# Performance work log

Hardware: AMD Instinct MI355X
Metric: run time of the kernel (lower is better)

The kernel has to match this reference:

```python
import jax, jax.numpy as jnp
import numpy as np

B, T, D, E = 4, 1024, 1024, 8
HD = 4 * D  # hdim = 4*dim


def setup_inputs() -> dict:
    key = jax.random.key(0)
    k1, k2, k3, k4 = jax.random.split(key, 4)
    std = 0.5 * D ** (-0.5)
    bound = (3.0 ** 0.5) * std
    x = jax.random.normal(k1, (B, T, D), dtype=jnp.float32)
    # router zero-init in source; use small random weights so routing is non-degenerate
    router_w = jax.random.normal(k2, (E, D), dtype=jnp.float32) * 0.02
    expert_fc = jax.random.uniform(k3, (E, D, HD), dtype=jnp.float32, minval=-bound, maxval=bound)
    # proj zero-init in source; use small random so output/backward are non-trivial
    expert_proj = jax.random.normal(k4, (E, D, HD), dtype=jnp.float32) * 0.02
    return {"x": x, "router_w": router_w, "expert_fc": expert_fc, "expert_proj": expert_proj}


def reference(x, router_w, expert_fc, expert_proj):
    # router: Linear(dim, E, bias=False) -> logits [B,T,E]
    logits = jnp.einsum('btd,ed->bte', x, router_w)
    probs = jax.nn.softmax(logits, axis=-1)
    expert_ids = jnp.argmax(probs, axis=-1)  # [B,T]; top-1 (max) routing
    # NOTE: source computes expert_weights (max prob) but does NOT use it in combine.
    mask = jax.nn.one_hot(expert_ids, E, dtype=x.dtype)  # [B,T,E]
    # Dense all-experts compute (faithful to source): h = x @ fc (F.linear with fc.T)
    h = jnp.einsum('btd,edh->ebth', x, expert_fc)
    h = jnp.square(jax.nn.relu(h))  # relu(h)**2
    # expert_output = h @ proj.T (F.linear with proj [dim, hdim])
    out_e = jnp.einsum('ebth,edh->ebtd', h, expert_proj)
    # masked combine: sum_e out_e * (ids == e)
    output = jnp.einsum('ebtd,bte->btd', out_e, mask)
    return output
```

## Files before the change

kernel.cpp:

```cpp
#include <hip/hip_runtime.h>
#include <hip/hip_bf16.h>
#include <stdint.h>

#define NE 8
#define DIM 1024
#define HDIM 4096
#define NTOK 4096
#define KSPLIT 4
#define MAXT 24
#define NT 16

typedef unsigned short ushort_t;
typedef __attribute__((ext_vector_type(4))) float f32x4;
typedef __attribute__((ext_vector_type(8))) short bf16x8;
typedef __attribute__((ext_vector_type(8))) ushort_t u16x8;

#define WAITV(n) asm volatile("s_waitcnt vmcnt(" #n ")" ::: "memory")
#define WAITL0() asm volatile("s_waitcnt lgkmcnt(0)" ::: "memory")
#define WAITL8() asm volatile("s_waitcnt lgkmcnt(8)" ::: "memory")
#define SCHEDB() __builtin_amdgcn_sched_barrier(0)
#define BARRIER() __builtin_amdgcn_s_barrier()

__device__ __forceinline__ ushort_t f2b(float f) {
  union { float f; unsigned u; } c; c.f = f;
  unsigned u = c.u;
  return (ushort_t)((u + 0x7fffu + ((u >> 16) & 1u)) >> 16);
}

__device__ __forceinline__ void gl2lds16(const void* g, void* l) {
  __builtin_amdgcn_global_load_lds(
      (__attribute__((address_space(1))) void*)g,
      (__attribute__((address_space(3))) void*)l, 16, 0, 0);
}

#define PH_MFMA(mh, nh)                                                     \
  { __builtin_amdgcn_s_setprio(1);                                          \
    _Pragma("unroll")                                                       \
    for (int i2 = 0; i2 < 4; ++i2) {                                        \
      _Pragma("unroll")                                                     \
      for (int j2 = 0; j2 < 2; ++j2) {                                      \
        _Pragma("unroll")                                                   \
        for (int kk = 0; kk < 2; ++kk)                                      \
          acc[(mh)*4 + i2][(nh)*2 + j2] =                                   \
            __builtin_amdgcn_mfma_f32_16x16x32_bf16(                        \
              af[i2][kk], bf[(nh)*2 + j2][kk],                              \
              acc[(mh)*4 + i2][(nh)*2 + j2], 0, 0, 0);                      \
      }                                                                     \
    }                                                                       \
    __builtin_amdgcn_s_setprio(0); }

#define LOAD_AF(mh)                                                         \
  { _Pragma("unroll")                                                       \
    for (int i2 = 0; i2 < 4; ++i2) {                                        \
      _Pragma("unroll")                                                     \
      for (int kk = 0; kk < 2; ++kk)                                        \
        af[i2][kk] = *(const bf16x8*)&pA[aBase + ((mh)*64 + i2*16)*64 + ck[kk]]; \
    } }
#define LOAD_BF(nh)                                                         \
  { _Pragma("unroll")                                                       \
    for (int j2 = 0; j2 < 2; ++j2) {                                        \
      _Pragma("unroll")                                                     \
      for (int kk = 0; kk < 2; ++kk)                                        \
        bf[(nh)*2 + j2][kk] = *(const bf16x8*)&pB[bBase + (((nh)*2 + j2)*16)*64 + ck[kk]]; \
    } }

__global__ __launch_bounds__(256) void router_kernel(
    const float* __restrict__ x, const float* __restrict__ rw,
    int* __restrict__ eid, int* __restrict__ rank, int* __restrict__ cnt) {
  __shared__ float w[NE * 1028];
  for (int i = threadIdx.x; i < NE * DIM; i += 256) {
    int e = i >> 10, d = i & 1023;
    w[e * 1028 + d] = rw[i];
  }
  __syncthreads();
  int grp = threadIdx.x >> 3;
  int e = threadIdx.x & 7;
  int t = blockIdx.x * 32 + grp;
  const float4* xr = (const float4*)(x + (size_t)t * DIM);
  const float4* wr = (const float4*)(w + e * 1028);
  float acc = 0.f;
#pragma unroll 4
  for (int i = 0; i < DIM / 4; ++i) {
    float4 xv = xr[i], wv = wr[i];
    acc += xv.x * wv.x + xv.y * wv.y + xv.z * wv.z + xv.w * wv.w;
  }
  float v = acc; int ie = e;
#pragma unroll
  for (int m = 4; m; m >>= 1) {
    float ov = __shfl_xor(v, m, 8);
    int oi = __shfl_xor(ie, m, 8);
    if (ov > v || (ov == v && oi < ie)) { v = ov; ie = oi; }
  }
  if (e == 0) {
    eid[t] = ie;
    rank[t] = atomicAdd(&cnt[ie], 1);
  }
}

__global__ void scan_kernel(const int* __restrict__ cnt, int* __restrict__ offs,
                            int* __restrict__ tile_e, int* __restrict__ tile_m,
                            int* __restrict__ ntiles) {
  if (threadIdx.x == 0) {
    int s = 0, nt = 0;
    for (int e = 0; e < NE; ++e) {
      offs[e] = s;
      int c = cnt[e];
      for (int m = 0; m < c; m += 256) { tile_e[nt] = e; tile_m[nt] = m; ++nt; }
      s += c;
    }
    offs[NE] = s;
    *ntiles = nt;
  }
}

__global__ __launch_bounds__(256) void gather_kernel(
    const float* __restrict__ x, const int* __restrict__ eid,
    const int* __restrict__ rank, const int* __restrict__ offs,
    int* __restrict__ sorted, ushort_t* __restrict__ Xg) {
  int t = blockIdx.x;
  int e = eid[t];
  int pos = offs[e] + rank[t];
  if (threadIdx.x == 0) sorted[pos] = t;
  int i = threadIdx.x;
  float4 v = ((const float4*)(x + (size_t)t * DIM))[i];
  ushort4 o = make_ushort4(f2b(v.x), f2b(v.y), f2b(v.z), f2b(v.w));
  *(ushort4*)(Xg + (size_t)pos * DIM + i * 4) = o;
}

__global__ __launch_bounds__(256) void transpose_fc_kernel(
    const float* __restrict__ fc, ushort_t* __restrict__ fct) {
  __shared__ float tile[64][68];
  int e = blockIdx.z;
  int h0 = blockIdx.x * 64, d0 = blockIdx.y * 64;
  int tid = threadIdx.x;
  int rr = tid >> 4;
  int cc = (tid & 15) * 4;
  const float* src = fc + ((size_t)e * DIM + d0 + rr) * HDIM + h0 + cc;
#pragma unroll
  for (int i = 0; i < 4; ++i) {
    float4 v = *(const float4*)(src + (size_t)(i * 16) * HDIM);
    *(float4*)&tile[rr + i * 16][cc] = v;
  }
  __syncthreads();
  int hr = tid >> 2;
  int dseg = (tid & 3) * 16;
  union { ushort_t s[16]; u16x8 v[2]; } o;
#pragma unroll
  for (int j = 0; j < 16; ++j) o.s[j] = f2b(tile[dseg + j][hr]);
  ushort_t* dst = fct + ((size_t)e * HDIM + h0 + hr) * DIM + d0 + dseg;
  *(u16x8*)dst = o.v[0];
  *(u16x8*)(dst + 8) = o.v[1];
}

__global__ __launch_bounds__(256) void cast_pj_kernel(
    const float* __restrict__ pj, ushort_t* __restrict__ pjb) {
  const size_t total = (size_t)NE * DIM * HDIM;
  size_t stride = (size_t)gridDim.x * 256 * 8;
  for (size_t i = ((size_t)blockIdx.x * 256 + threadIdx.x) * 8; i < total; i += stride) {
    f32x4 a = *(const f32x4*)(pj + i);
    f32x4 b = *(const f32x4*)(pj + i + 4);
    union { ushort_t s[8]; u16x8 v; } o;
    o.s[0] = f2b(a[0]); o.s[1] = f2b(a[1]); o.s[2] = f2b(a[2]); o.s[3] = f2b(a[3]);
    o.s[4] = f2b(b[0]); o.s[5] = f2b(b[1]); o.s[6] = f2b(b[2]); o.s[7] = f2b(b[3]);
    *(u16x8*)(pjb + i) = o.v;
  }
}

#define GEMM_MAIN_LOOP()                                                    \
  stB(0, 0, 0); stB(0, 0, 1); stA(0, 0, 0); stA(0, 0, 1);                   \
  stB(1, 1, 0); stB(1, 1, 1); stA(1, 1, 0);                                 \
  WAITV(6);                                                                 \
  BARRIER();                                                                \
  _Pragma("unroll 1")                                                       \
  for (int T = 0; T < NT; T += 2) {                                         \
    { const ushort_t* pA = As[0]; const ushort_t* pB = Bs[0];               \
                                                                   \
      LOAD_AF(0); LOAD_BF(0);                                               \
      stA(1, T + 1, 1);                                                     \
      WAITL8(); SCHEDB();                                                   \
      BARRIER(); WAITL0(); SCHEDB();                                        \
      PH_MFMA(0, 0);                                                        \
      BARRIER();                                                            \
                                                                   \
      LOAD_BF(1);                                                           \
      BARRIER(); WAITL0(); SCHEDB();                                        \
      PH_MFMA(0, 1);                                                        \
      BARRIER();                                                            \
                                                                   \
      LOAD_AF(1);                                                           \
      if (T + 2 < NT) stB(0, T + 2, 0);                                     \
      BARRIER(); WAITL0(); SCHEDB();                                        \
      PH_MFMA(1, 0);                                                        \
      BARRIER();                                                            \
                                                                   \
      if (T + 2 < NT) { stB(0, T + 2, 1); stA(0, T + 2, 0); WAITV(6); }     \
      else            { WAITV(0); }                                         \
      BARRIER(); SCHEDB();                                                  \
      PH_MFMA(1, 1);                                                        \
      BARRIER();                                                            \
    }                                                                       \
    { const ushort_t* pA = As[1]; const ushort_t* pB = Bs[1];               \
                                                                   \
      LOAD_AF(0); LOAD_BF(0);                                               \
      if (T + 2 < NT) stA(0, T + 2, 1);                                     \
      WAITL8(); SCHEDB();                                                   \
      BARRIER(); WAITL0(); SCHEDB();                                        \
      PH_MFMA(0, 0);                                                        \
      BARRIER();                                                            \
                                                                   \
      LOAD_BF(1);                                                           \
      BARRIER(); WAITL0(); SCHEDB();                                        \
      PH_MFMA(0, 1);                                                        \
      BARRIER();                                                            \
                                                                   \
      LOAD_AF(1);                                                           \
      if (T + 3 < NT) stB(1, T + 3, 0);                                     \
      BARRIER(); WAITL0(); SCHEDB();                                        \
      PH_MFMA(1, 0);                                                        \
      BARRIER();                                                            \
                                                                   \
      if (T + 3 < NT) { stB(1, T + 3, 1); stA(1, T + 3, 0); WAITV(6); }     \
      BARRIER(); SCHEDB();                                                  \
      PH_MFMA(1, 1);                                                        \
      BARRIER();                                                            \
    }                                                                       \
  }

__global__ __launch_bounds__(512, 2) void gemm1_kernel(
    const ushort_t* __restrict__ Xg, const ushort_t* __restrict__ fct,
    const int* __restrict__ offs, const int* __restrict__ tile_e,
    const int* __restrict__ tile_m, const int* __restrict__ ntiles,
    ushort_t* __restrict__ H) {
  __shared__ ushort_t As[2][16384];
  __shared__ ushort_t Bs[2][16384];

  int lin = blockIdx.x + 16 * blockIdx.y;
  int sw = (lin & 7) * 48 + (lin >> 3);
  int bx = sw & 15, by = sw >> 4;
  if (by >= *ntiles) return;

  int e = tile_e[by];
  int mb = tile_m[by];
  int m0 = offs[e];
  int Me = offs[e + 1] - m0;
  int n0 = bx * 256;

  int tid = threadIdx.x;
  int wave = tid >> 6;
  int lane = tid & 63;
  int fr = lane & 15, kq = lane >> 4;
  int wr = wave & 1, wc = wave >> 1;

  int swk = ((tid & 7) ^ ((tid >> 3) & 7)) * 8;
  const ushort_t* aSrc[4]; const ushort_t* bSrc[4];
#pragma unroll
  for (int c = 0; c < 4; ++c) {
    int r = c * 64 + (tid >> 3);
    int rg = mb + r; if (rg >= Me) rg = Me - 1;
    aSrc[c] = Xg + (size_t)(m0 + rg) * DIM + swk;
    bSrc[c] = fct + ((size_t)e * HDIM + n0 + r) * DIM + swk;
  }
  int sdst = wave * 512;

  int aBase = (wr * 128 + fr) * 64;
  int bBase = (wc * 64 + fr) * 64;
  int ck[2] = { (kq ^ (fr & 7)) * 8, ((4 + kq) ^ (fr & 7)) * 8 };

  f32x4 acc[8][4] = {};
  bf16x8 af[4][2], bf[4][2];

  auto stA = [&](int p, int X, int h) __attribute__((always_inline)) {
    int ko = X * 64;
    gl2lds16(aSrc[2 * h] + ko,     &As[p][(2 * h) * 4096 + sdst]);
    gl2lds16(aSrc[2 * h + 1] + ko, &As[p][(2 * h + 1) * 4096 + sdst]);
  };
  auto stB = [&](int p, int X, int h) __attribute__((always_inline)) {
    int ko = X * 64;
    gl2lds16(bSrc[2 * h] + ko,     &Bs[p][(2 * h) * 4096 + sdst]);
    gl2lds16(bSrc[2 * h + 1] + ko, &Bs[p][(2 * h + 1) * 4096 + sdst]);
  };

  GEMM_MAIN_LOOP();

  int cq = kq * 4;
#pragma unroll
  for (int i = 0; i < 8; ++i) {
#pragma unroll
    for (int r = 0; r < 4; ++r) {
      int rl = wr * 128 + i * 16 + cq + r;
      int rg = mb + rl;
      if (rg < Me) {
        ushort_t* dst = H + (size_t)(m0 + rg) * HDIM + n0 + wc * 64 + fr;
#pragma unroll
        for (int j = 0; j < 4; ++j) {
          float v = acc[i][j][r];
          v = fmaxf(v, 0.f);
          dst[j * 16] = f2b(v * v);
        }
      }
    }
  }
}

__global__ __launch_bounds__(512, 2) void gemm2_kernel(
    const ushort_t* __restrict__ Hm, const ushort_t* __restrict__ pjb,
    const int* __restrict__ offs, const int* __restrict__ tile_e,
    const int* __restrict__ tile_m, const int* __restrict__ ntiles,
    const int* __restrict__ sorted, float* P, float* __restrict__ out) {
  __shared__ ushort_t As[2][16384];
  __shared__ ushort_t Bs[2][16384];

  int lin = blockIdx.x + 4 * (blockIdx.y + MAXT * blockIdx.z);
  int sw = (lin & 7) * 48 + (lin >> 3);
  int bx = sw & 3;
  int t2 = sw >> 2;
  int by = t2 % MAXT, bz = t2 / MAXT;
  if (by >= *ntiles) return;

  int e = tile_e[by];
  int mb = tile_m[by];
  int ks = bz;
  int m0 = offs[e];
  int Me = offs[e + 1] - m0;
  int n0 = bx * 256;
  int kbeg = ks * (HDIM / KSPLIT);

  int tid = threadIdx.x;
  int wave = tid >> 6;
  int lane = tid & 63;
  int fr = lane & 15, kq = lane >> 4;
  int wr = wave & 1, wc = wave >> 1;

  int swk = ((tid & 7) ^ ((tid >> 3) & 7)) * 8;
  const ushort_t* aSrc[4]; const ushort_t* bSrc[4];
#pragma unroll
  for (int c = 0; c < 4; ++c) {
    int r = c * 64 + (tid >> 3);
    int rg = mb + r; if (rg >= Me) rg = Me - 1;
    aSrc[c] = Hm + (size_t)(m0 + rg) * HDIM + kbeg + swk;
    bSrc[c] = pjb + ((size_t)e * DIM + n0 + r) * HDIM + kbeg + swk;
  }
  int sdst = wave * 512;

  int aBase = (wr * 128 + fr) * 64;
  int bBase = (wc * 64 + fr) * 64;
  int ck[2] = { (kq ^ (fr & 7)) * 8, ((4 + kq) ^ (fr & 7)) * 8 };

  f32x4 acc[8][4] = {};
  bf16x8 af[4][2], bf[4][2];

  auto stA = [&](int p, int X, int h) __attribute__((always_inline)) {
    int ko = X * 64;
    gl2lds16(aSrc[2 * h] + ko,     &As[p][(2 * h) * 4096 + sdst]);
    gl2lds16(aSrc[2 * h + 1] + ko, &As[p][(2 * h + 1) * 4096 + sdst]);
  };
  auto stB = [&](int p, int X, int h) __attribute__((always_inline)) {
    int ko = X * 64;
    gl2lds16(bSrc[2 * h] + ko,     &Bs[p][(2 * h) * 4096 + sdst]);
    gl2lds16(bSrc[2 * h + 1] + ko, &Bs[p][(2 * h + 1) * 4096 + sdst]);
  };

  GEMM_MAIN_LOOP();

  int cq = kq * 4;
  if (P) {
#pragma unroll
    for (int i = 0; i < 8; ++i) {
#pragma unroll
      for (int r = 0; r < 4; ++r) {
        int rl = wr * 128 + i * 16 + cq + r;
        int rg = mb + rl;
        if (rg < Me) {
          float* dst = P + ((size_t)ks * NTOK + (m0 + rg)) * DIM + n0 + wc * 64 + fr;
#pragma unroll
          for (int j = 0; j < 4; ++j) dst[j * 16] = acc[i][j][r];
        }
      }
    }
  } else {
#pragma unroll
    for (int i = 0; i < 8; ++i) {
#pragma unroll
      for (int r = 0; r < 4; ++r) {
        int rl = wr * 128 + i * 16 + cq + r;
        int rg = mb + rl;
        if (rg < Me) {
          int tok = sorted[m0 + rg];
          float* dst = out + (size_t)tok * DIM + n0 + wc * 64 + fr;
#pragma unroll
          for (int j = 0; j < 4; ++j) atomicAdd(&dst[j * 16], acc[i][j][r]);
        }
      }
    }
  }
}

__global__ __launch_bounds__(256) void reduce_kernel(
    const float* __restrict__ P, const int* __restrict__ sorted,
    float* __restrict__ out) {
  int pos = blockIdx.x;
  int tok = sorted[pos];
  int i = threadIdx.x;
  size_t base = (size_t)pos * DIM + i * 4;
  const size_t S = (size_t)NTOK * DIM;
  f32x4 s = *(const f32x4*)(P + base) + *(const f32x4*)(P + S + base) +
            *(const f32x4*)(P + 2 * S + base) + *(const f32x4*)(P + 3 * S + base);
  *(f32x4*)(out + (size_t)tok * DIM + i * 4) = s;
}

extern "C" void kernel_launch(void* const* d_in, const int* in_sizes, int n_in,
                              void* d_out, int out_size, void* d_ws, size_t ws_size,
                              hipStream_t stream) {
  const float* x  = (const float*)d_in[0];
  const float* rw = (const float*)d_in[1];
  const float* fc = (const float*)d_in[2];
  const float* pj = (const float*)d_in[3];
  float* out = (float*)d_out;
  char* ws = (char*)d_ws;

  int* eid        = (int*)(ws + 0x0000);
  int* rank       = (int*)(ws + 0x4000);
  int* cnt        = (int*)(ws + 0x8000);
  int* offs       = (int*)(ws + 0x8100);
  int* tile_e     = (int*)(ws + 0x8200);
  int* tile_m     = (int*)(ws + 0x8600);
  int* ntiles     = (int*)(ws + 0x8a00);
  int* sorted     = (int*)(ws + 0x9000);
  ushort_t* Xg    = (ushort_t*)(ws + 0x10000);
  ushort_t* H     = (ushort_t*)(ws + 0x810000);
  ushort_t* W     = (ushort_t*)(ws + 0x2810000);

  const size_t pOff = 0x6810000ULL;
  const size_t pBytes = (size_t)KSPLIT * NTOK * DIM * sizeof(float);
  bool bigws = ws_size >= pOff + pBytes;
  float* P = bigws ? (float*)(ws + pOff) : nullptr;

  hipMemsetAsync(cnt, 0, 32, stream);
  if (!bigws) hipMemsetAsync(out, 0, (size_t)NTOK * DIM * sizeof(float), stream);
  router_kernel<<<NTOK / 32, 256, 0, stream>>>(x, rw, eid, rank, cnt);
  scan_kernel<<<1, 64, 0, stream>>>(cnt, offs, tile_e, tile_m, ntiles);
  gather_kernel<<<NTOK, 256, 0, stream>>>(x, eid, rank, offs, sorted, Xg);
  transpose_fc_kernel<<<dim3(HDIM / 64, DIM / 64, NE), 256, 0, stream>>>(fc, W);
  gemm1_kernel<<<dim3(HDIM / 256, MAXT), 512, 0, stream>>>(Xg, W, offs, tile_e, tile_m, ntiles, H);
  cast_pj_kernel<<<4096, 256, 0, stream>>>(pj, W);
  gemm2_kernel<<<dim3(DIM / 256, MAXT, KSPLIT), 512, 0, stream>>>(
      H, W, offs, tile_e, tile_m, ntiles, sorted, P, out);
  if (bigws) reduce_kernel<<<NTOK, 256, 0, stream>>>(P, sorted, out);
}
```

Before: 503.7 us.

## Fuse fp32-to-bf16 proj cast into gemm2 loads and use atomic split-K combine

```diff
diff --git a/kernel.cpp b/kernel.cpp
--- a/kernel.cpp
+++ b/kernel.cpp
@@ -152,20 +152,6 @@
   *(u16x8*)(dst + 8) = o.v[1];
 }
 
-__global__ __launch_bounds__(256) void cast_pj_kernel(
-    const float* __restrict__ pj, ushort_t* __restrict__ pjb) {
-  const size_t total = (size_t)NE * DIM * HDIM;
-  size_t stride = (size_t)gridDim.x * 256 * 8;
-  for (size_t i = ((size_t)blockIdx.x * 256 + threadIdx.x) * 8; i < total; i += stride) {
-    f32x4 a = *(const f32x4*)(pj + i);
-    f32x4 b = *(const f32x4*)(pj + i + 4);
-    union { ushort_t s[8]; u16x8 v; } o;
-    o.s[0] = f2b(a[0]); o.s[1] = f2b(a[1]); o.s[2] = f2b(a[2]); o.s[3] = f2b(a[3]);
-    o.s[4] = f2b(b[0]); o.s[5] = f2b(b[1]); o.s[6] = f2b(b[2]); o.s[7] = f2b(b[3]);
-    *(u16x8*)(pjb + i) = o.v;
-  }
-}
-
 #define GEMM_MAIN_LOOP()                                                    \
   stB(0, 0, 0); stB(0, 0, 1); stA(0, 0, 0); stA(0, 0, 1);                   \
   stB(1, 1, 0); stB(1, 1, 1); stA(1, 1, 0);                                 \
@@ -303,10 +289,10 @@
 }
 
 __global__ __launch_bounds__(512, 2) void gemm2_kernel(
-    const ushort_t* __restrict__ Hm, const ushort_t* __restrict__ pjb,
+    const ushort_t* __restrict__ Hm, const float* __restrict__ pj,
     const int* __restrict__ offs, const int* __restrict__ tile_e,
     const int* __restrict__ tile_m, const int* __restrict__ ntiles,
-    const int* __restrict__ sorted, float* P, float* __restrict__ out) {
+    const int* __restrict__ sorted, float* __restrict__ out) {
   __shared__ ushort_t As[2][16384];
   __shared__ ushort_t Bs[2][16384];
 
@@ -332,15 +318,22 @@
   int wr = wave & 1, wc = wave >> 1;
 
   int swk = ((tid & 7) ^ ((tid >> 3) & 7)) * 8;
-  const ushort_t* aSrc[4]; const ushort_t* bSrc[4];
+  const ushort_t* aSrc[4];
 #pragma unroll
   for (int c = 0; c < 4; ++c) {
     int r = c * 64 + (tid >> 3);
     int rg = mb + r; if (rg >= Me) rg = Me - 1;
     aSrc[c] = Hm + (size_t)(m0 + rg) * HDIM + kbeg + swk;
-    bSrc[c] = pjb + ((size_t)e * DIM + n0 + r) * HDIM + kbeg + swk;
   }
   int sdst = wave * 512;
+
+  int brow = tid >> 1;
+  int bc0 = (tid & 1) * 4;
+  const float* bSrcBase = pj + ((size_t)e * DIM + n0 + brow) * HDIM + kbeg + bc0 * 8;
+  int bOff[4];
+#pragma unroll
+  for (int j2 = 0; j2 < 4; ++j2)
+    bOff[j2] = brow * 64 + ((bc0 + j2) ^ (brow & 7)) * 8;
 
   int aBase = (wr * 128 + fr) * 64;
   int bBase = (wc * 64 + fr) * 64;
@@ -348,64 +341,103 @@
 
   f32x4 acc[8][4] = {};
   bf16x8 af[4][2], bf[4][2];
-
-  auto stA = [&](int p, int X, int h) __attribute__((always_inline)) {
+  float4 bv[8];
+
+  auto loadB = [&](int X) __attribute__((always_inline)) {
+    const float* s = bSrcBase + X * 64;
+#pragma unroll
+    for (int j = 0; j < 8; ++j) bv[j] = *(const float4*)(s + j * 4);
+  };
+  auto writeB = [&](int pb) __attribute__((always_inline)) {
+#pragma unroll
+    for (int j2 = 0; j2 < 4; ++j2) {
+      union { unsigned u[4]; bf16x8 v; } w;
+      float4 a = bv[2 * j2], b = bv[2 * j2 + 1];
+      w.u[0] = (unsigned)f2b(a.x) | ((unsigned)f2b(a.y) << 16);
+      w.u[1] = (unsigned)f2b(a.z) | ((unsigned)f2b(a.w) << 16);
+      w.u[2] = (unsigned)f2b(b.x) | ((unsigned)f2b(b.y) << 16);
+      w.u[3] = (unsigned)f2b(b.z) | ((unsigned)f2b(b.w) << 16);
+      *(bf16x8*)&Bs[pb][bOff[j2]] = w.v;
+    }
+  };
+  auto stA4 = [&](int p, int X) __attribute__((always_inline)) {
     int ko = X * 64;
-    gl2lds16(aSrc[2 * h] + ko,     &As[p][(2 * h) * 4096 + sdst]);
-    gl2lds16(aSrc[2 * h + 1] + ko, &As[p][(2 * h + 1) * 4096 + sdst]);
+#pragma unroll
+    for (int c = 0; c < 4; ++c)
+      gl2lds16(aSrc[c] + ko, &As[p][c * 4096 + sdst]);
   };
-  auto stB = [&](int p, int X, int h) __attribute__((always_inline)) {
-    int ko = X * 64;
-    gl2lds16(bSrc[2 * h] + ko,     &Bs[p][(2 * h) * 4096 + sdst]);
-    gl2lds16(bSrc[2 * h + 1] + ko, &Bs[p][(2 * h + 1) * 4096 + sdst]);
-  };
-
-  GEMM_MAIN_LOOP();
+
+  loadB(0);
+  stA4(0, 0);
+  WAITV(4);
+  writeB(0);
+  loadB(1);
+  stA4(1, 1);
+  WAITV(12);
+  WAITL0();
+  BARRIER();
+
+#pragma unroll 1
+  for (int T = 0; T < NT; T += 2) {
+    const bool more = (T + 2 < NT);
+    { const ushort_t* pA = As[0]; const ushort_t* pB = Bs[0];
+      WAITV(4);
+      writeB(1);
+      if (more) loadB(T + 2);
+      LOAD_AF(0); LOAD_BF(0);
+      BARRIER(); WAITL0(); SCHEDB();
+      PH_MFMA(0, 0);
+      BARRIER();
+      LOAD_BF(1);
+      BARRIER(); WAITL0(); SCHEDB();
+      PH_MFMA(0, 1);
+      BARRIER();
+      LOAD_AF(1);
+      BARRIER(); WAITL0(); SCHEDB();
+      PH_MFMA(1, 0);
+      BARRIER();
+      if (more) { stA4(0, T + 2); WAITV(8); }
+      else      { WAITV(0); }
+      BARRIER(); SCHEDB();
+      PH_MFMA(1, 1);
+      BARRIER();
+    }
+    { const ushort_t* pA = As[1]; const ushort_t* pB = Bs[1];
+      if (more) { WAITV(4); writeB(0); loadB(T + 3); }
+      LOAD_AF(0); LOAD_BF(0);
+      BARRIER(); WAITL0(); SCHEDB();
+      PH_MFMA(0, 0);
+      BARRIER();
+      LOAD_BF(1);
+      BARRIER(); WAITL0(); SCHEDB();
+      PH_MFMA(0, 1);
+      BARRIER();
+      LOAD_AF(1);
+      BARRIER(); WAITL0(); SCHEDB();
+      PH_MFMA(1, 0);
+      BARRIER();
+      if (more) { stA4(1, T + 3); WAITV(8); }
+      BARRIER(); SCHEDB();
+      PH_MFMA(1, 1);
+      BARRIER();
+    }
+  }
 
   int cq = kq * 4;
-  if (P) {
-#pragma unroll
-    for (int i = 0; i < 8; ++i) {
-#pragma unroll
-      for (int r = 0; r < 4; ++r) {
-        int rl = wr * 128 + i * 16 + cq + r;
-        int rg = mb + rl;
-        if (rg < Me) {
-          float* dst = P + ((size_t)ks * NTOK + (m0 + rg)) * DIM + n0 + wc * 64 + fr;
-#pragma unroll
-          for (int j = 0; j < 4; ++j) dst[j * 16] = acc[i][j][r];
-        }
+#pragma unroll
+  for (int i = 0; i < 8; ++i) {
+#pragma unroll
+    for (int r = 0; r < 4; ++r) {
+      int rl = wr * 128 + i * 16 + cq + r;
+      int rg = mb + rl;
+      if (rg < Me) {
+        int tok = sorted[m0 + rg];
+        float* dst = out + (size_t)tok * DIM + n0 + wc * 64 + fr;
+#pragma unroll
+        for (int j = 0; j < 4; ++j) atomicAdd(&dst[j * 16], acc[i][j][r]);
       }
     }
-  } else {
-#pragma unroll
-    for (int i = 0; i < 8; ++i) {
-#pragma unroll
-      for (int r = 0; r < 4; ++r) {
-        int rl = wr * 128 + i * 16 + cq + r;
-        int rg = mb + rl;
-        if (rg < Me) {
-          int tok = sorted[m0 + rg];
-          float* dst = out + (size_t)tok * DIM + n0 + wc * 64 + fr;
-#pragma unroll
-          for (int j = 0; j < 4; ++j) atomicAdd(&dst[j * 16], acc[i][j][r]);
-        }
-      }
-    }
-  }
-}
-
-__global__ __launch_bounds__(256) void reduce_kernel(
-    const float* __restrict__ P, const int* __restrict__ sorted,
-    float* __restrict__ out) {
-  int pos = blockIdx.x;
-  int tok = sorted[pos];
-  int i = threadIdx.x;
-  size_t base = (size_t)pos * DIM + i * 4;
-  const size_t S = (size_t)NTOK * DIM;
-  f32x4 s = *(const f32x4*)(P + base) + *(const f32x4*)(P + S + base) +
-            *(const f32x4*)(P + 2 * S + base) + *(const f32x4*)(P + 3 * S + base);
-  *(f32x4*)(out + (size_t)tok * DIM + i * 4) = s;
+  }
 }
 
 extern "C" void kernel_launch(void* const* d_in, const int* in_sizes, int n_in,
@@ -430,20 +462,13 @@
   ushort_t* H     = (ushort_t*)(ws + 0x810000);
   ushort_t* W     = (ushort_t*)(ws + 0x2810000);
 
-  const size_t pOff = 0x6810000ULL;
-  const size_t pBytes = (size_t)KSPLIT * NTOK * DIM * sizeof(float);
-  bool bigws = ws_size >= pOff + pBytes;
-  float* P = bigws ? (float*)(ws + pOff) : nullptr;
-
   hipMemsetAsync(cnt, 0, 32, stream);
-  if (!bigws) hipMemsetAsync(out, 0, (size_t)NTOK * DIM * sizeof(float), stream);
+  hipMemsetAsync(out, 0, (size_t)NTOK * DIM * sizeof(float), stream);
   router_kernel<<<NTOK / 32, 256, 0, stream>>>(x, rw, eid, rank, cnt);
   scan_kernel<<<1, 64, 0, stream>>>(cnt, offs, tile_e, tile_m, ntiles);
   gather_kernel<<<NTOK, 256, 0, stream>>>(x, eid, rank, offs, sorted, Xg);
   transpose_fc_kernel<<<dim3(HDIM / 64, DIM / 64, NE), 256, 0, stream>>>(fc, W);
   gemm1_kernel<<<dim3(HDIM / 256, MAXT), 512, 0, stream>>>(Xg, W, offs, tile_e, tile_m, ntiles, H);
-  cast_pj_kernel<<<4096, 256, 0, stream>>>(pj, W);
   gemm2_kernel<<<dim3(DIM / 256, MAXT, KSPLIT), 512, 0, stream>>>(
-      H, W, offs, tile_e, tile_m, ntiles, sorted, P, out);
-  if (bigws) reduce_kernel<<<NTOK, 256, 0, stream>>>(P, sorted, out);
-}
+      H, pj, offs, tile_e, tile_m, ntiles, sorted, out);
+}
```

Result: slower. 575.3 us (+14.2%).
